# Optimization experiments

Hardware: AMD Instinct MI355X
Metric: run time of the kernel (lower is better)

## Reference

```python
import jax, jax.numpy as jnp
import numpy as np

V, B, C, H, W, D, G = 5, 1, 32, 384, 384, 4, 8


def _rot(a, b, c):
    ca, sa = np.cos(a), np.sin(a)
    cb, sb = np.cos(b), np.sin(b)
    cc, sc = np.cos(c), np.sin(c)
    Rx = np.array([[1, 0, 0], [0, ca, -sa], [0, sa, ca]])
    Ry = np.array([[cb, 0, sb], [0, 1, 0], [-sb, 0, cb]])
    Rz = np.array([[cc, -sc, 0], [sc, cc, 0], [0, 0, 1]])
    return (Rz @ Ry @ Rx).astype(np.float32)


def setup_inputs():
    key = jax.random.key(0)
    ks = jax.random.split(key, 8)
    features = jax.random.normal(ks[0], (V, B, C, H, W), jnp.float32)
    current_depths = jax.random.uniform(ks[1], (B, D, H, W), jnp.float32, 425.0, 935.0)
    rng = np.random.RandomState(0)
    Ks = np.zeros((B, V, 3, 3), np.float32)
    Es = np.zeros((B, V, 3, 4), np.float32)
    for b in range(B):
        for v in range(V):
            f = 0.8 * W * (1.0 + 0.01 * rng.randn())
            Ks[b, v] = np.array([[f, 0, W / 2.0], [0, f, H / 2.0], [0, 0, 1.0]], np.float32)
            if v == 0:
                Rm = np.eye(3, dtype=np.float32)
                t = np.zeros(3, np.float32)
            else:
                Rm = _rot(*(0.02 * rng.randn(3)))
                t = np.array([25.0 * v, 5.0 * rng.randn(), 5.0 * rng.randn()], np.float32)
            Es[b, v, :, :3] = Rm
            Es[b, v, :, 3] = t
    w0 = 0.3 * jax.random.normal(ks[2], (16, G), jnp.float32)
    b0 = jnp.zeros((16,), jnp.float32)
    w1 = 0.3 * jax.random.normal(ks[3], (8, 16), jnp.float32)
    b1 = jnp.zeros((8,), jnp.float32)
    w2 = 0.3 * jax.random.normal(ks[4], (1, 8), jnp.float32)
    b2 = jnp.zeros((1,), jnp.float32)
    return {"features": features, "current_depths": current_depths,
            "cam_intrinsic": jnp.asarray(Ks), "cam_extrinsic": jnp.asarray(Es),
            "w0": w0, "b0": b0, "w1": w1, "b1": b1, "w2": w2, "b2": b2}


def _bilinear_sample(feat, px, py):
    # feat [B,C,H,W]; px,py [B,N] pixel coords (align_corners=True), zero padding
    Bn, Cn, Hn, Wn = feat.shape
    ff = feat.reshape(Bn, Cn, Hn * Wn)
    x0 = jnp.floor(px)
    y0 = jnp.floor(py)
    wx1 = px - x0
    wx0 = 1.0 - wx1
    wy1 = py - y0
    wy0 = 1.0 - wy1

    def gather(xi, yi, w):
        valid = (xi >= 0) & (xi <= Wn - 1) & (yi >= 0) & (yi <= Hn - 1)
        xc = jnp.clip(xi, 0, Wn - 1).astype(jnp.int32)
        yc = jnp.clip(yi, 0, Hn - 1).astype(jnp.int32)
        idx = yc * Wn + xc  # [B,N]
        v = jnp.take_along_axis(ff, idx[:, None, :], axis=2)  # [B,C,N]
        return v * (w * valid)[:, None, :]

    return (gather(x0, y0, wx0 * wy0) + gather(x0 + 1.0, y0, wx1 * wy0)
            + gather(x0, y0 + 1.0, wx0 * wy1) + gather(x0 + 1.0, y0 + 1.0, wx1 * wy1))


def _pixelwise_net(sim, w0, b0, w1, b1, w2, b2):
    # PixelwiseNet: 1x1x1 Conv3d G->16->8->1 (BN folded to identity, eval stats), sigmoid, max over depth
    x = jax.nn.relu(jnp.einsum('og,bgdhw->bodhw', w0, sim) + b0[None, :, None, None, None])
    x = jax.nn.relu(jnp.einsum('oc,bcdhw->bodhw', w1, x) + b1[None, :, None, None, None])
    x = jnp.einsum('oc,bcdhw->bodhw', w2, x) + b2[None, :, None, None, None]
    return jnp.max(jax.nn.sigmoid(x), axis=2)  # [B,1,H,W]


def reference(features, current_depths, cam_intrinsic, cam_extrinsic, w0, b0, w1, b1, w2, b2):
    ref_feat = features[0]                                   # [B,C,H,W]
    ref_g = ref_feat.reshape(B, G, C // G, H, W)
    # pixel grid with half-pixel centers, homogeneous [3, H*W]
    xs = jnp.arange(W, dtype=jnp.float32) + 0.5
    ys = jnp.arange(H, dtype=jnp.float32) + 0.5
    gx, gy = jnp.meshgrid(xs, ys)                            # [H,W]
    grid = jnp.stack([gx.ravel(), gy.ravel(), jnp.ones(H * W, jnp.float32)], 0)
    K_ref_inv = jnp.linalg.inv(cam_intrinsic[:, 0])          # [B,3,3]
    R = cam_extrinsic[:, :, :3, :3]                          # [B,V,3,3]
    t = cam_extrinsic[:, :, :3, 3:4]                         # [B,V,3,1]
    R_ref_inv = jnp.linalg.inv(R[:, 0])                      # [B,3,3]
    uv = jnp.einsum('bij,jn->bin', K_ref_inv, grid)          # [B,3,HW]
    cam_pts = uv[:, None] * current_depths.reshape(B, D, 1, H * W)   # [B,D,3,HW]
    world = jnp.einsum('bij,bdjn->bdin', R_ref_inv, cam_pts - t[:, 0:1])
    world = world.transpose(0, 2, 1, 3).reshape(B, 3, D * H * W)     # [B,3,N], N=D*H*W
    sim_sum = 0.0
    w_sum = 0.0
    for s in range(1, V):
        cp = jnp.einsum('bij,bjn->bin', R[:, s], world) + t[:, s]    # [B,3,N]
        uvd = jnp.einsum('bij,bjn->bin', cam_intrinsic[:, s], cp)
        z = uvd[:, 2] + 1e-9
        px = uvd[:, 0] / z
        py = uvd[:, 1] / z
        warped = _bilinear_sample(features[s], px, py)               # [B,C,N]
        warped = warped.reshape(B, G, C // G, D, H, W)
        sim = jnp.mean(warped * ref_g[:, :, :, None], axis=2)        # [B,G,D,H,W]
        vw = _pixelwise_net(sim, w0, b0, w1, b1, w2, b2)             # [B,1,H,W]
        sim_sum = sim_sum + sim * vw[:, :, None]
        w_sum = w_sum + vw[:, :, None]
    return sim_sum / w_sum
```

## Files before the change

### kernel.cpp

```cpp
#include <hip/hip_runtime.h>
#include <math.h>

#define Vn 5
#define Cn 32
#define Hn 384
#define Wn 384
#define Dn 4
#define Gn 8
#define HWn (Hn*Wn)

typedef _Float16 h2 __attribute__((ext_vector_type(2)));

__device__ __forceinline__ float fdot2h(h2 a, h2 b, float c){
#if __has_builtin(__builtin_amdgcn_fdot2)
    return __builtin_amdgcn_fdot2(a, b, c, false);
#else
    return (float)a.x*(float)b.x + (float)a.y*(float)b.y + c;
#endif
}
__device__ __forceinline__ unsigned int packh2(float a, float b){
    h2 h;
    h.x = (_Float16)a;
    h.y = (_Float16)b;
    return __builtin_bit_cast(unsigned int, h);
}

__device__ __forceinline__ void inv3(const float* m, float* o){
    float a=m[0],b=m[1],c=m[2],d=m[3],e=m[4],f=m[5],g=m[6],h=m[7],i=m[8];
    float A =  e*i - f*h;
    float B = -(d*i - f*g);
    float C =  d*h - e*g;
    float det = a*A + b*B + c*C;
    float r = 1.f/det;
    o[0] = A*r;            o[1] = -(b*i - c*h)*r;  o[2] =  (b*f - c*e)*r;
    o[3] = B*r;            o[4] =  (a*i - c*g)*r;  o[5] = -(a*f - c*d)*r;
    o[6] = C*r;            o[7] = -(a*h - b*g)*r;  o[8] =  (a*e - b*d)*r;
}
__device__ __forceinline__ void mm3(const float* a, const float* b, float* o){
    #pragma unroll
    for (int r=0;r<3;r++)
        #pragma unroll
        for (int c=0;c<3;c++)
            o[r*3+c] = a[r*3+0]*b[0*3+c] + a[r*3+1]*b[1*3+c] + a[r*3+2]*b[2*3+c];
}
__device__ __forceinline__ void mv3(const float* a, const float* v, float* o){
    #pragma unroll
    for (int r=0;r<3;r++)
        o[r] = a[r*3+0]*v[0] + a[r*3+1]*v[1] + a[r*3+2]*v[2];
}

__global__ __launch_bounds__(256)
void transpose_kernel(const float* __restrict__ feat, unsigned short* __restrict__ featT){
    __shared__ float tile[32][257];
    const int s  = blockIdx.y;
    const int p0 = blockIdx.x * 256;
    const int t  = threadIdx.x;
    const float* src = feat + (size_t)(s+1)*Cn*HWn + p0;
    #pragma unroll
    for (int k=0;k<8;k++){
        const int i   = k*256 + t;
        const int px4 = (i & 63) * 4;
        const int ch  = i >> 6;
        const float4 v = *(const float4*)(src + (size_t)ch*HWn + px4);
        tile[ch][px4+0]=v.x; tile[ch][px4+1]=v.y; tile[ch][px4+2]=v.z; tile[ch][px4+3]=v.w;
    }
    __syncthreads();
    uint4* dst = (uint4*)(featT + ((size_t)s*HWn + p0 + t)*Cn);
    #pragma unroll
    for (int q=0;q<4;q++){
        uint4 o;
        o.x = packh2(tile[8*q+0][t], tile[8*q+1][t]);
        o.y = packh2(tile[8*q+2][t], tile[8*q+3][t]);
        o.z = packh2(tile[8*q+4][t], tile[8*q+5][t]);
        o.w = packh2(tile[8*q+6][t], tile[8*q+7][t]);
        dst[q] = o;
    }
}

#define DOTG(uA, uB, g)                                                        \
    {                                                                          \
        const h2 pa = __builtin_bit_cast(h2, (uA));                            \
        const h2 pb = __builtin_bit_cast(h2, (uB));                            \
        const float dt = fdot2h(pa, r2[2*(g)], fdot2h(pb, r2[2*(g)+1], 0.f));  \
        sg[(g)] = fmaf(w, dt, sg[(g)]);                                        \
    }

__device__ __forceinline__ void tap_f16(const unsigned short* __restrict__ vbase,
                                        int xc, int yc, float w,
                                        const h2* r2, float* sg)
{
    if (w != 0.f){
        const uint4* p = (const uint4*)(vbase + ((size_t)yc*Wn + xc)*Cn);
        const uint4 q0 = p[0];
        const uint4 q1 = p[1];
        const uint4 q2 = p[2];
        const uint4 q3 = p[3];
        DOTG(q0.x, q0.y, 0)
        DOTG(q0.z, q0.w, 1)
        DOTG(q1.x, q1.y, 2)
        DOTG(q1.z, q1.w, 3)
        DOTG(q2.x, q2.y, 4)
        DOTG(q2.z, q2.w, 5)
        DOTG(q3.x, q3.y, 6)
        DOTG(q3.z, q3.w, 7)
    }
}

__global__ __launch_bounds__(256, 2)
void gbinet_kernel(const float* __restrict__ feat,
                   const float* __restrict__ depths,
                   const float* __restrict__ Kin,
                   const float* __restrict__ Ein,
                   const float* __restrict__ w0, const float* __restrict__ b0,
                   const float* __restrict__ w1, const float* __restrict__ b1,
                   const float* __restrict__ w2, const float* __restrict__ b2,
                   const unsigned short* __restrict__ featT,
                   float* __restrict__ out)
{
    __shared__ float sW0[128], sW1[128], sB0[16], sB1[8], sW2[8], sB2s[1];
    __shared__ float sM[48];
    __shared__ float sRef[64*33];
    __shared__ float sDep[4*65];
    __shared__ float sOut[64*33];
    const int t = threadIdx.x;
    if (t < 128){ sW0[t] = w0[t]; sW1[t] = w1[t]; }
    if (t < 16) sB0[t] = b0[t];
    if (t < 8){ sB1[t] = b1[t]; sW2[t] = w2[t]; }

    const int bid = blockIdx.x;
    const int sid = (bid & 7) * (HWn/64/8) + (bid >> 3);
    const int blockBase = sid * 64;

    {
        const float* srcR = feat + blockBase;
        #pragma unroll
        for (int k=0;k<8;k++){
            const int i  = k*256 + t;
            const int c  = i >> 6;
            const int px = i & 63;
            sRef[px*33 + c] = srcR[(size_t)c*HWn + px];
        }
        const int dp = t >> 6;
        const int px = t & 63;
        sDep[dp*65 + px] = depths[(size_t)dp*HWn + blockBase + px];
    }

    if (t == 0){
        sB2s[0] = b2[0];
        float K0inv[9]; inv3(Kin, K0inv);
        float R0[9], t0[3];
        #pragma unroll
        for (int r=0;r<3;r++){
            #pragma unroll
            for (int c=0;c<3;c++) R0[r*3+c] = Ein[r*4+c];
            t0[r] = Ein[r*4+3];
        }
        float R0inv[9]; inv3(R0, R0inv);
        float M0[9]; mm3(R0inv, K0inv, M0);
        float Rt0[3]; mv3(R0inv, t0, Rt0);
        for (int s=1;s<Vn;s++){
            const float* Ks = Kin + s*9;
            const float* Es = Ein + s*12;
            float Rs[9], ts[3];
            #pragma unroll
            for (int r=0;r<3;r++){
                #pragma unroll
                for (int c=0;c<3;c++) Rs[r*3+c] = Es[r*4+c];
                ts[r] = Es[r*4+3];
            }
            float T1[9]; mm3(Rs, M0, T1);
            float A[9];  mm3(Ks, T1, A);
            float Rr[3]; mv3(Rs, Rt0, Rr);
            float tv[3] = { ts[0]-Rr[0], ts[1]-Rr[1], ts[2]-Rr[2] };
            float cv[3]; mv3(Ks, tv, cv);
            float* dm = &sM[(s-1)*12];
            #pragma unroll
            for (int i=0;i<9;i++) dm[i] = A[i];
            #pragma unroll
            for (int i=0;i<3;i++) dm[9+i] = cv[i];
        }
    }
    __syncthreads();

    const int pixLocal = t >> 2;
    const int s        = t & 3;
    const int pix      = blockBase + pixLocal;
    const float xg = (float)(pix % Wn) + 0.5f;
    const float yg = (float)(pix / Wn) + 0.5f;

    h2 r2[16];
    #pragma unroll
    for (int k=0;k<16;k++){
        r2[k].x = (_Float16)sRef[pixLocal*33 + 2*k];
        r2[k].y = (_Float16)sRef[pixLocal*33 + 2*k+1];
    }
    float dep[Dn];
    #pragma unroll
    for (int d=0;d<Dn;d++) dep[d] = sDep[d*65 + pixLocal];

    const float* M = &sM[s*12];
    const float bx = M[0]*xg + M[1]*yg + M[2];
    const float by = M[3]*xg + M[4]*yg + M[5];
    const float bz = M[6]*xg + M[7]*yg + M[8];
    const float cx = M[9], cy = M[10], cz = M[11];
    const unsigned short* vbase = featT + (size_t)s*HWn*Cn;

    float sim[Gn][Dn];
    #pragma unroll
    for (int d=0;d<Dn;d++){
        const float dd = dep[d];
        const float ux = fmaf(bx, dd, cx);
        const float uy = fmaf(by, dd, cy);
        const float uz = fmaf(bz, dd, cz) + 1e-9f;
        const float rz = 1.f/uz;
        const float px = ux*rz, py = uy*rz;
        const float x0 = floorf(px), y0 = floorf(py);
        const float wx1 = px - x0, wy1 = py - y0;
        const float wx0 = 1.f - wx1, wy0 = 1.f - wy1;
        const bool vx0 = (x0 >= 0.f)     && (x0 <= (float)(Wn-1));
        const bool vx1 = (x0 >= -1.f)    && (x0 <= (float)(Wn-2));
        const bool vy0 = (y0 >= 0.f)     && (y0 <= (float)(Hn-1));
        const bool vy1 = (y0 >= -1.f)    && (y0 <= (float)(Hn-2));
        const float w00 = (vx0&&vy0) ? 0.25f*wx0*wy0 : 0.f;
        const float w10 = (vx1&&vy0) ? 0.25f*wx1*wy0 : 0.f;
        const float w01 = (vx0&&vy1) ? 0.25f*wx0*wy1 : 0.f;
        const float w11 = (vx1&&vy1) ? 0.25f*wx1*wy1 : 0.f;
        const int xi0 = (int)fminf(fmaxf(x0,     0.f), (float)(Wn-1));
        const int xi1 = (int)fminf(fmaxf(x0+1.f, 0.f), (float)(Wn-1));
        const int yi0 = (int)fminf(fmaxf(y0,     0.f), (float)(Hn-1));
        const int yi1 = (int)fminf(fmaxf(y0+1.f, 0.f), (float)(Hn-1));

        float sg[Gn];
        #pragma unroll
        for (int g=0; g<Gn; g++) sg[g] = 0.f;
        tap_f16(vbase, xi0, yi0, w00, r2, sg);
        tap_f16(vbase, xi1, yi0, w10, r2, sg);
        tap_f16(vbase, xi0, yi1, w01, r2, sg);
        tap_f16(vbase, xi1, yi1, w11, r2, sg);
        #pragma unroll
        for (int g=0; g<Gn; g++) sim[g][d] = sg[g];
    }

    float maxlog = -3.0e38f;
    #pragma unroll
    for (int dp=0; dp<2; dp++){
        const int d0 = 2*dp, d1 = 2*dp+1;
        float hx[16], hy[16];
        #pragma unroll
        for (int o=0;o<16;o++){
            float ax = sB0[o], ay = sB0[o];
            #pragma unroll
            for (int g=0; g<Gn; g++){
                const float wv = sW0[o*Gn+g];
                ax = fmaf(wv, sim[g][d0], ax);
                ay = fmaf(wv, sim[g][d1], ay);
            }
            hx[o] = fmaxf(ax, 0.f);
            hy[o] = fmaxf(ay, 0.f);
        }
        float lgx = sB2s[0], lgy = sB2s[0];
        #pragma unroll
        for (int o=0;o<8;o++){
            float ax = sB1[o], ay = sB1[o];
            #pragma unroll
            for (int i=0;i<16;i++){
                const float wv = sW1[o*16+i];
                ax = fmaf(wv, hx[i], ax);
                ay = fmaf(wv, hy[i], ay);
            }
            const float w2v = sW2[o];
            lgx = fmaf(w2v, fmaxf(ax, 0.f), lgx);
            lgy = fmaf(w2v, fmaxf(ay, 0.f), lgy);
        }
        maxlog = fmaxf(maxlog, fmaxf(lgx, lgy));
    }
    const float vw = 1.f/(1.f + __expf(-maxlog));

    float wsum = vw;
    wsum += __shfl_xor(wsum, 1);
    wsum += __shfl_xor(wsum, 2);
    #pragma unroll
    for (int g=0;g<Gn;g++)
        #pragma unroll
        for (int d=0;d<Dn;d++){
            float v = sim[g][d]*vw;
            v += __shfl_xor(v, 1);
            v += __shfl_xor(v, 2);
            sim[g][d] = v;
        }

    if (s == 0){
        const float invw = 1.f/wsum;
        #pragma unroll
        for (int g=0;g<Gn;g++)
            #pragma unroll
            for (int d=0;d<Dn;d++)
                sOut[pixLocal*33 + g*Dn + d] = sim[g][d]*invw;
    }
    __syncthreads();

    float* oBase = out + blockBase;
    #pragma unroll
    for (int k=0;k<8;k++){
        const int e     = k*256 + t;
        const int plane = e >> 6;
        const int pixel = e & 63;
        oBase[(size_t)plane*HWn + pixel] = sOut[pixel*33 + plane];
    }
}

extern "C" void kernel_launch(void* const* d_in, const int* in_sizes, int n_in,
                              void* d_out, int out_size, void* d_ws, size_t ws_size,
                              hipStream_t stream)
{
    (void)in_sizes; (void)n_in; (void)out_size; (void)ws_size;
    const float* feat   = (const float*)d_in[0];
    const float* depths = (const float*)d_in[1];
    const float* K      = (const float*)d_in[2];
    const float* E      = (const float*)d_in[3];
    const float* w0     = (const float*)d_in[4];
    const float* b0     = (const float*)d_in[5];
    const float* w1     = (const float*)d_in[6];
    const float* b1     = (const float*)d_in[7];
    const float* w2     = (const float*)d_in[8];
    const float* b2     = (const float*)d_in[9];
    float* out = (float*)d_out;
    unsigned short* featT = (unsigned short*)d_ws;

    dim3 g(HWn/256, Vn-1);
    transpose_kernel<<<g, 256, 0, stream>>>(feat, featT);
    gbinet_kernel<<<HWn/64, 256, 0, stream>>>(feat, depths, K, E,
                                              w0,b0,w1,b1,w2,b2, featT, out);
}
```

Baseline: 237.6 us.

## Register-only fp16 transpose and unconditional batched loads of all four bilinear taps

The transpose kernel drops its shared-memory tile. Each thread now reads float4 runs across all 32 channels for 4 pixels, packs them to fp16 in registers and writes 64-byte channel-last records, so each block covers 1024 pixels. In the sampling loop, the four taps' 64-byte loads are all issued up front without the zero-weight branch, so memory latency can overlap across taps. The cost is extra loads for out-of-bounds taps (zero-weighted but clamped to valid addresses), higher register pressure in the main kernel, and less coalesced writes in the transpose.

```diff
diff --git a/kernel.cpp b/kernel.cpp
--- a/kernel.cpp
+++ b/kernel.cpp
@@ -51,60 +51,51 @@
 
 __global__ __launch_bounds__(256)
 void transpose_kernel(const float* __restrict__ feat, unsigned short* __restrict__ featT){
-    __shared__ float tile[32][257];
     const int s  = blockIdx.y;
-    const int p0 = blockIdx.x * 256;
-    const int t  = threadIdx.x;
+    const int p0 = blockIdx.x * 1024 + threadIdx.x * 4;
     const float* src = feat + (size_t)(s+1)*Cn*HWn + p0;
-    #pragma unroll
-    for (int k=0;k<8;k++){
-        const int i   = k*256 + t;
-        const int px4 = (i & 63) * 4;
-        const int ch  = i >> 6;
-        const float4 v = *(const float4*)(src + (size_t)ch*HWn + px4);
-        tile[ch][px4+0]=v.x; tile[ch][px4+1]=v.y; tile[ch][px4+2]=v.z; tile[ch][px4+3]=v.w;
-    }
-    __syncthreads();
-    uint4* dst = (uint4*)(featT + ((size_t)s*HWn + p0 + t)*Cn);
-    #pragma unroll
-    for (int q=0;q<4;q++){
-        uint4 o;
-        o.x = packh2(tile[8*q+0][t], tile[8*q+1][t]);
-        o.y = packh2(tile[8*q+2][t], tile[8*q+3][t]);
-        o.z = packh2(tile[8*q+4][t], tile[8*q+5][t]);
-        o.w = packh2(tile[8*q+6][t], tile[8*q+7][t]);
-        dst[q] = o;
-    }
-}
-
-#define DOTG(uA, uB, g)                                                        \
+    unsigned int outw[4][16];
+    #pragma unroll
+    for (int c=0; c<Cn; c+=2){
+        const float4 a = *(const float4*)(src + (size_t)c*HWn);
+        const float4 b = *(const float4*)(src + (size_t)(c+1)*HWn);
+        outw[0][c>>1] = packh2(a.x, b.x);
+        outw[1][c>>1] = packh2(a.y, b.y);
+        outw[2][c>>1] = packh2(a.z, b.z);
+        outw[3][c>>1] = packh2(a.w, b.w);
+    }
+    uint4* dst = (uint4*)(featT + ((size_t)s*HWn + p0)*Cn);
+    #pragma unroll
+    for (int p=0;p<4;p++){
+        #pragma unroll
+        for (int q=0;q<4;q++){
+            uint4 o;
+            o.x = outw[p][4*q+0];
+            o.y = outw[p][4*q+1];
+            o.z = outw[p][4*q+2];
+            o.w = outw[p][4*q+3];
+            dst[p*4+q] = o;
+        }
+    }
+}
+
+#define DOTG(uA, uB, g, WV)                                                    \
     {                                                                          \
         const h2 pa = __builtin_bit_cast(h2, (uA));                            \
         const h2 pb = __builtin_bit_cast(h2, (uB));                            \
         const float dt = fdot2h(pa, r2[2*(g)], fdot2h(pb, r2[2*(g)+1], 0.f));  \
-        sg[(g)] = fmaf(w, dt, sg[(g)]);                                        \
-    }
-
-__device__ __forceinline__ void tap_f16(const unsigned short* __restrict__ vbase,
-                                        int xc, int yc, float w,
-                                        const h2* r2, float* sg)
-{
-    if (w != 0.f){
-        const uint4* p = (const uint4*)(vbase + ((size_t)yc*Wn + xc)*Cn);
-        const uint4 q0 = p[0];
-        const uint4 q1 = p[1];
-        const uint4 q2 = p[2];
-        const uint4 q3 = p[3];
-        DOTG(q0.x, q0.y, 0)
-        DOTG(q0.z, q0.w, 1)
-        DOTG(q1.x, q1.y, 2)
-        DOTG(q1.z, q1.w, 3)
-        DOTG(q2.x, q2.y, 4)
-        DOTG(q2.z, q2.w, 5)
-        DOTG(q3.x, q3.y, 6)
-        DOTG(q3.z, q3.w, 7)
-    }
-}
+        sg[(g)] = fmaf((WV), dt, sg[(g)]);                                     \
+    }
+
+#define TAPDOT(Q0, Q1, Q2, Q3, WT)                                             \
+    DOTG((Q0).x, (Q0).y, 0, WT)                                                \
+    DOTG((Q0).z, (Q0).w, 1, WT)                                                \
+    DOTG((Q1).x, (Q1).y, 2, WT)                                                \
+    DOTG((Q1).z, (Q1).w, 3, WT)                                                \
+    DOTG((Q2).x, (Q2).y, 4, WT)                                                \
+    DOTG((Q2).z, (Q2).w, 5, WT)                                                \
+    DOTG((Q3).x, (Q3).y, 6, WT)                                                \
+    DOTG((Q3).z, (Q3).w, 7, WT)
 
 __global__ __launch_bounds__(256, 2)
 void gbinet_kernel(const float* __restrict__ feat,
@@ -230,13 +221,22 @@
         const int yi0 = (int)fminf(fmaxf(y0,     0.f), (float)(Hn-1));
         const int yi1 = (int)fminf(fmaxf(y0+1.f, 0.f), (float)(Hn-1));
 
+        const uint4* pA = (const uint4*)(vbase + ((size_t)yi0*Wn + xi0)*Cn);
+        const uint4* pB = (const uint4*)(vbase + ((size_t)yi0*Wn + xi1)*Cn);
+        const uint4* pC = (const uint4*)(vbase + ((size_t)yi1*Wn + xi0)*Cn);
+        const uint4* pD = (const uint4*)(vbase + ((size_t)yi1*Wn + xi1)*Cn);
+        const uint4 A0 = pA[0], A1 = pA[1], A2 = pA[2], A3 = pA[3];
+        const uint4 B0 = pB[0], B1 = pB[1], B2 = pB[2], B3 = pB[3];
+        const uint4 C0 = pC[0], C1 = pC[1], C2 = pC[2], C3 = pC[3];
+        const uint4 D0 = pD[0], D1 = pD[1], D2 = pD[2], D3 = pD[3];
+
         float sg[Gn];
         #pragma unroll
         for (int g=0; g<Gn; g++) sg[g] = 0.f;
-        tap_f16(vbase, xi0, yi0, w00, r2, sg);
-        tap_f16(vbase, xi1, yi0, w10, r2, sg);
-        tap_f16(vbase, xi0, yi1, w01, r2, sg);
-        tap_f16(vbase, xi1, yi1, w11, r2, sg);
+        TAPDOT(A0, A1, A2, A3, w00)
+        TAPDOT(B0, B1, B2, B3, w10)
+        TAPDOT(C0, C1, C2, C3, w01)
+        TAPDOT(D0, D1, D2, D3, w11)
         #pragma unroll
         for (int g=0; g<Gn; g++) sim[g][d] = sg[g];
     }
@@ -327,7 +327,7 @@
     float* out = (float*)d_out;
     unsigned short* featT = (unsigned short*)d_ws;
 
-    dim3 g(HWn/256, Vn-1);
+    dim3 g(HWn/1024, Vn-1);
     transpose_kernel<<<g, 256, 0, stream>>>(feat, featT);
     gbinet_kernel<<<HWn/64, 256, 0, stream>>>(feat, depths, K, E,
                                               w0,b0,w1,b1,w2,b2, featT, out);
```

After: 276.8 us. 1.16x slower.
